# Kernel tuning notes

Measured on AMD Instinct MI355X. Metric: run time of the kernel, lower is better.

## Reference

```python
import jax, jax.numpy as jnp
import numpy as np

B, D_IN, D_BOT, C = 8192, 2048, 1024, 1000
SHARE = 500          # cfg.share_class_num
TEMP = 0.05          # cfg.temp
NEG_FILL = -1e9
EPS = 1e-12          # F.normalize eps


def setup_inputs() -> dict:
    key = jax.random.key(0)
    ks = jax.random.split(key, 6)
    return {
        "features": jax.random.normal(ks[0], (B, D_IN), jnp.float32),
        "W_b": jax.random.normal(ks[1], (D_BOT, D_IN), jnp.float32) * 0.02,
        "b_b": jnp.zeros((D_BOT,), jnp.float32),
        "W1": jax.random.normal(ks[2], (C, D_BOT), jnp.float32) * 0.02,
        "W2": jax.random.normal(ks[3], (C, D_BOT), jnp.float32) * 0.02,
        "centroid": jax.random.normal(ks[4], (C, D_BOT), jnp.float32) * 0.02,
    }


def mask_mechanism(outputs):
    # per-row mask: argmax -> row mask -> masked softmax (branchless)
    predict = jnp.argmax(outputs, axis=1)                       # [B]
    cls = jnp.arange(C)                                          # [C]
    base = cls < SHARE                                           # shared classes masked
    # if predicted class is private (>= SHARE), mask the whole row ...
    row_mask = jnp.where((predict >= SHARE)[:, None], True, base[None, :])
    # ... but always unmask the predicted class itself
    row_mask = row_mask & (cls[None, :] != predict[:, None])     # [B, C] bool
    masked = jnp.where(row_mask, jnp.float32(NEG_FILL), outputs)
    return jax.nn.softmax(masked, axis=1)


def reference(features, W_b, b_b, W1, W2, centroid):
    feats = features @ W_b.T + b_b                               # bottleneck [B, D_BOT]
    outputs1 = feats @ W1.T                                      # [B, C]
    sm1 = mask_mechanism(outputs1)
    feat_oa = sm1 @ centroid                                     # [B, D_BOT]
    features_aug = feats + feat_oa
    # F.normalize(dim=1): x / max(||x||_2, eps)
    norm = jnp.sqrt(jnp.sum(features_aug * features_aug, axis=1, keepdims=True))
    x = features_aug / jnp.maximum(norm, EPS)
    outputs2 = (x @ W2.T) / TEMP                                 # [B, C]
    softmax_outputs = jax.nn.softmax(outputs2, axis=1)
    return (feats, features_aug, outputs1, outputs2, softmax_outputs)
```

## Files before the change

kernel.cpp:

```cpp
#include <hip/hip_runtime.h>
#include <cmath>


typedef _Float16 h8 __attribute__((ext_vector_type(8)));
typedef _Float16 h4 __attribute__((ext_vector_type(4)));
typedef float f32x4 __attribute__((ext_vector_type(4)));

#define TAU 0.015f
#define CAP 1024

__device__ __forceinline__ void gload_lds16(const _Float16* g, _Float16* l) {
    __builtin_amdgcn_global_load_lds(
        (const __attribute__((address_space(1))) void*)g,
        (__attribute__((address_space(3))) void*)l, 16, 0, 0);
}

__global__ void zero_cnt_kernel(int* __restrict__ cnt) { *cnt = 0; }

template <int MODE>
__global__ __launch_bounds__(256, (MODE >= 5) ? 2 : 4) void gemm16(
    const _Float16* __restrict__ Ah, const _Float16* __restrict__ Al, int lda,
    const _Float16* __restrict__ Bh, const _Float16* __restrict__ Bl, int ldb,
    int klen,
    float* __restrict__ C, int ldc, int nC,
    const float* __restrict__ aux,
    _Float16* __restrict__ Ch,
    const int* __restrict__ cnt)
{
    constexpr bool P2 = (MODE >= 5);
    __shared__ _Float16 sAh[128 * 64];
    __shared__ _Float16 sBh[128 * 64];
    __shared__ _Float16 sAl[P2 ? 128 * 64 : 8];
    __shared__ _Float16 sBl[P2 ? 128 * 64 : 8];

    const int t = threadIdx.x;
    const int lane = t & 63, wid = t >> 6;
    int row0, col0, kbase;
    if constexpr (MODE >= 5) {
        row0 = blockIdx.y * 128; col0 = blockIdx.x * 128;
        kbase = blockIdx.z * klen;
        if (row0 >= *cnt) return;
    } else {
        const int wg = blockIdx.x;
        const int wgid = (wg & 7) * 64 + (wg >> 3);
        row0 = (wgid >> 3) * 128; col0 = (wgid & 7) * 128;
        kbase = 0;
    }
    const int wr = wid >> 1, wc = wid & 1;
    const int fr = lane & 15;
    const int fk = (lane >> 4) * 8;
    const int srow = lane >> 3;
    const int scol = (lane & 7) * 8;

    f32x4 acc[4][4] = {};
    f32x4 accc[4][4] = {};

    for (int k0 = kbase; k0 < kbase + klen; k0 += 64) {
        #pragma unroll
        for (int j = 0; j < 4; ++j) {
            int i = wid * 4 + j;
            int r = i * 8 + srow;
            const size_t ga = (size_t)(row0 + r) * lda + k0 + scol;
            const size_t gb = (size_t)(col0 + r) * ldb + k0 + scol;
            gload_lds16(Ah + ga, &sAh[i * 512]);
            gload_lds16(Bh + gb, &sBh[i * 512]);
            if constexpr (P2) {
                gload_lds16(Al + ga, &sAl[i * 512]);
                gload_lds16(Bl + gb, &sBl[i * 512]);
            }
        }
        __syncthreads();
        #pragma unroll
        for (int ks = 0; ks < 2; ++ks) {
            h8 ah[4], al[4];
            #pragma unroll
            for (int mf = 0; mf < 4; ++mf) {
                int rr = wr * 64 + mf * 16 + fr;
                ah[mf] = *(const h8*)&sAh[rr * 64 + ks * 32 + fk];
                if constexpr (P2) al[mf] = *(const h8*)&sAl[rr * 64 + ks * 32 + fk];
            }
            #pragma unroll
            for (int nf = 0; nf < 4; ++nf) {
                int cc = wc * 64 + nf * 16 + fr;
                h8 bh = *(const h8*)&sBh[cc * 64 + ks * 32 + fk];
                h8 bl;
                if constexpr (P2) bl = *(const h8*)&sBl[cc * 64 + ks * 32 + fk];
                #pragma unroll
                for (int mf = 0; mf < 4; ++mf) {
                    acc[mf][nf] = __builtin_amdgcn_mfma_f32_16x16x32_f16(ah[mf], bh, acc[mf][nf], 0, 0, 0);
                    if constexpr (P2) {
                        accc[mf][nf] = __builtin_amdgcn_mfma_f32_16x16x32_f16(ah[mf], bl, accc[mf][nf], 0, 0, 0);
                        accc[mf][nf] = __builtin_amdgcn_mfma_f32_16x16x32_f16(al[mf], bh, accc[mf][nf], 0, 0, 0);
                    }
                }
            }
        }
        __syncthreads();
    }
    float* Cz = C;
    if constexpr (MODE >= 5) Cz = C + (size_t)blockIdx.z * CAP * ldc;
    #pragma unroll
    for (int mf = 0; mf < 4; ++mf) {
        #pragma unroll
        for (int nf = 0; nf < 4; ++nf) {
            f32x4 v = acc[mf][nf];
            if constexpr (P2) v = v + accc[mf][nf] * (1.0f / 2048.0f);
            const int gcol = col0 + wc * 64 + nf * 16 + fr;
            const int rbase = row0 + wr * 64 + mf * 16 + (lane >> 4) * 4;
            #pragma unroll
            for (int j = 0; j < 4; ++j) {
                const int grow = rbase + j;
                float val = v[j];
                if constexpr (MODE == 1) val += aux[gcol];
                if constexpr (MODE == 3) val += aux[(size_t)grow * 1024 + gcol];
                if constexpr (MODE == 4) val *= 20.0f;
                if (gcol < nC) {
                    Cz[(size_t)grow * ldc + gcol] = val;
                    if constexpr (MODE == 1)
                        Ch[(size_t)grow * 1024 + gcol] = (_Float16)val;
                }
            }
        }
    }
}

__global__ void conv_kernel(const float* __restrict__ src, _Float16* __restrict__ hi, int n4)
{
    for (int i = blockIdx.x * 256 + threadIdx.x; i < n4; i += gridDim.x * 256) {
        f32x4 v = ((const f32x4*)src)[i];
        h4 h;
        #pragma unroll
        for (int j = 0; j < 4; ++j) h[j] = (_Float16)v[j];
        ((h4*)hi)[i] = h;
    }
}

__global__ void split_kernel(const float* __restrict__ src,
                             _Float16* __restrict__ hi, _Float16* __restrict__ lo, int n4)
{
    for (int i = blockIdx.x * 256 + threadIdx.x; i < n4; i += gridDim.x * 256) {
        f32x4 v = ((const f32x4*)src)[i];
        h4 h, l;
        #pragma unroll
        for (int j = 0; j < 4; ++j) {
            _Float16 hh = (_Float16)v[j];
            h[j] = hh;
            l[j] = (_Float16)((v[j] - (float)hh) * 2048.0f);
        }
        ((h4*)hi)[i] = h;
        ((h4*)lo)[i] = l;
    }
}

template <bool LO>
__global__ void padsplit_kernel(const float* __restrict__ src,
                                _Float16* __restrict__ hi, _Float16* __restrict__ lo, int nrows)
{
    for (int i = blockIdx.x * 256 + threadIdx.x; i < 1024 * 256; i += gridDim.x * 256) {
        int r = i >> 8;
        f32x4 v = {0.f, 0.f, 0.f, 0.f};
        if (r < nrows) v = ((const f32x4*)src)[i];
        h4 h, l;
        #pragma unroll
        for (int j = 0; j < 4; ++j) {
            _Float16 hh = (_Float16)v[j];
            h[j] = hh;
            if constexpr (LO) l[j] = (_Float16)((v[j] - (float)hh) * 2048.0f);
        }
        ((h4*)hi)[i] = h;
        if constexpr (LO) ((h4*)lo)[i] = l;
    }
}

__global__ __launch_bounds__(256) void ctrans_kernel(const float* __restrict__ centroid,
                                                     _Float16* __restrict__ cT)
{
    __shared__ float tile[32][33];
    const int t = threadIdx.x;
    const int tx = t & 31, ty = t >> 5;
    const int k0 = blockIdx.y * 32, n0 = blockIdx.x * 32;
    #pragma unroll
    for (int p = 0; p < 4; ++p) {
        int k = k0 + ty + p * 8;
        tile[ty + p * 8][tx] = (k < 1000) ? centroid[(size_t)k * 1024 + n0 + tx] : 0.0f;
    }
    __syncthreads();
    #pragma unroll
    for (int p = 0; p < 4; ++p) {
        int n = n0 + ty + p * 8;
        cT[(size_t)n * 1024 + k0 + tx] = (_Float16)tile[tx][ty + p * 8];
    }
}

__device__ __forceinline__ void masked_softmax_body(
    const float* __restrict__ x, _Float16* __restrict__ y,
    int t, float* wv, int* wi, bool flag, int* d_idx, int* d_cnt, int rowid)
{
    float bv = -1e30f, sv = -1e30f; int bi = 0;
    for (int c = t; c < 1000; c += 256) {
        float v = x[c];
        if (v > bv) { sv = bv; bv = v; bi = c; }
        else if (v > sv) sv = v;
    }
    #pragma unroll
    for (int off = 32; off > 0; off >>= 1) {
        float ov = __shfl_down(bv, off, 64);
        int   oi = __shfl_down(bi, off, 64);
        float os = __shfl_down(sv, off, 64);
        if (ov > bv || (ov == bv && oi < bi)) {
            sv = fmaxf(bv, os); bv = ov; bi = oi;
        } else {
            sv = fmaxf(sv, fmaxf(ov, os) == ov ? ov : os);
            sv = fmaxf(sv, ov); sv = fmaxf(sv, os);
        }
    }
    __shared__ float svv[4];
    const int lane = t & 63, wid = t >> 6;
    if (lane == 0) { wv[wid] = bv; wi[wid] = bi; svv[wid] = sv; }
    __syncthreads();
    __shared__ float s_m, s_tot; __shared__ int s_p;
    if (t == 0) {
        float mv = wv[0]; int mi = wi[0]; float m2 = svv[0];
        for (int w = 1; w < 4; ++w) {
            if (wv[w] > mv || (wv[w] == mv && wi[w] < mi)) {
                m2 = fmaxf(mv, svv[w]); mv = wv[w]; mi = wi[w];
            } else {
                m2 = fmaxf(m2, fmaxf(wv[w], svv[w]));
            }
        }
        s_p = mi; s_m = mv;
        if (flag && (mv - m2) < TAU) {
            int slot = atomicAdd(d_cnt, 1);
            if (slot < CAP) d_idx[slot] = rowid;
        }
    }
    __syncthreads();
    const int p = s_p; const float m = s_m;
    if (p >= 500) {
        for (int c = t; c < 1024; c += 256) y[c] = (c == p) ? (_Float16)1.0f : (_Float16)0.0f;
    } else {
        float s = 0.f;
        for (int c = t; c < 1000; c += 256)
            if (c == p || c >= 500) s += expf(x[c] - m);
        #pragma unroll
        for (int off = 32; off > 0; off >>= 1) s += __shfl_down(s, off, 64);
        if (lane == 0) wv[wid] = s;
        __syncthreads();
        if (t == 0) s_tot = wv[0] + wv[1] + wv[2] + wv[3];
        __syncthreads();
        const float inv = 1.0f / s_tot;
        for (int c = t; c < 1024; c += 256) {
            float v = 0.f;
            if (c < 1000 && (c == p || c >= 500)) v = expf(x[c] - m) * inv;
            y[c] = (_Float16)v;
        }
    }
}

__global__ __launch_bounds__(256) void masksm_kernel(const float* __restrict__ o1,
                                                     _Float16* __restrict__ sm,
                                                     int* __restrict__ d_idx,
                                                     int* __restrict__ d_cnt)
{
    __shared__ float wv[4]; __shared__ int wi[4];
    const int row = blockIdx.x;
    masked_softmax_body(o1 + (size_t)row * 1000, sm + (size_t)row * 1024,
                        threadIdx.x, wv, wi, true, d_idx, d_cnt, row);
}

__global__ __launch_bounds__(256) void fixup_kernel(const float* __restrict__ o1g,
                                                    _Float16* __restrict__ sm,
                                                    const int* __restrict__ d_idx,
                                                    const int* __restrict__ d_cnt)
{
    const int slot = blockIdx.x;
    if (slot >= *d_cnt || slot >= CAP) return;
    const int row = d_idx[slot];
    __shared__ float wv[4]; __shared__ int wi[4];
    masked_softmax_body(o1g + (size_t)slot * 1000, sm + (size_t)row * 1024,
                        threadIdx.x, wv, wi, false, nullptr, nullptr, 0);
}

__global__ __launch_bounds__(256) void gather_split_kernel(
    const float* __restrict__ features,
    _Float16* __restrict__ fgh, _Float16* __restrict__ fgl,
    const int* __restrict__ d_idx, const int* __restrict__ d_cnt)
{
    const int slot = blockIdx.x;
    if (slot >= *d_cnt || slot >= CAP) return;
    const int row = d_idx[slot];
    const int t = threadIdx.x;
    #pragma unroll
    for (int q = 0; q < 2; ++q) {
        int o = t * 8 + q * 4;
        f32x4 v = *(const f32x4*)(features + (size_t)row * 2048 + o);
        h4 h, l;
        #pragma unroll
        for (int j = 0; j < 4; ++j) {
            _Float16 hh = (_Float16)v[j];
            h[j] = hh;
            l[j] = (_Float16)((v[j] - (float)hh) * 2048.0f);
        }
        *(h4*)(fgh + (size_t)slot * 2048 + o) = h;
        *(h4*)(fgl + (size_t)slot * 2048 + o) = l;
    }
}

__global__ __launch_bounds__(256) void red1_kernel(const float* __restrict__ P1,
                                                   const float* __restrict__ bias,
                                                   _Float16* __restrict__ fgsh,
                                                   _Float16* __restrict__ fgsl,
                                                   const int* __restrict__ d_cnt)
{
    const int slot = blockIdx.x;
    if (slot >= *d_cnt || slot >= CAP) return;
    const int t = threadIdx.x;
    #pragma unroll
    for (int q = 0; q < 4; ++q) {
        const int c = t + q * 256;
        const size_t o = (size_t)slot * 1024 + c;
        float s = P1[o] + P1[o + (size_t)CAP * 1024] + P1[o + (size_t)2 * CAP * 1024]
                + P1[o + (size_t)3 * CAP * 1024] + bias[c];
        _Float16 h = (_Float16)s;
        fgsh[o] = h;
        fgsl[o] = (_Float16)((s - (float)h) * 2048.0f);
    }
}

__global__ __launch_bounds__(256) void red2_kernel(const float* __restrict__ P2,
                                                   float* __restrict__ o1g,
                                                   const int* __restrict__ d_cnt)
{
    const int slot = blockIdx.x;
    if (slot >= *d_cnt || slot >= CAP) return;
    const int t = threadIdx.x;
    for (int c = t; c < 1000; c += 256) {
        const size_t o = (size_t)slot * 1000 + c;
        o1g[o] = P2[o] + P2[o + (size_t)CAP * 1000];
    }
}

__global__ __launch_bounds__(256) void rownorm_x_kernel(const float* __restrict__ aug,
                                                        _Float16* __restrict__ xh)
{
    const int row = blockIdx.x; const int t = threadIdx.x;
    f32x4 v = *((const f32x4*)(aug + (size_t)row * 1024) + t);
    float s = v[0]*v[0] + v[1]*v[1] + v[2]*v[2] + v[3]*v[3];
    #pragma unroll
    for (int off = 32; off > 0; off >>= 1) s += __shfl_down(s, off, 64);
    __shared__ float ws4[4]; __shared__ float s_inv;
    const int lane = t & 63, wid = t >> 6;
    if (lane == 0) ws4[wid] = s;
    __syncthreads();
    if (t == 0) {
        float tot = ws4[0] + ws4[1] + ws4[2] + ws4[3];
        s_inv = 1.0f / fmaxf(sqrtf(tot), 1e-12f);
    }
    __syncthreads();
    const float inv = s_inv;
    h4 h;
    #pragma unroll
    for (int j = 0; j < 4; ++j) h[j] = (_Float16)(v[j] * inv);
    *((h4*)(xh + (size_t)row * 1024) + t) = h;
}

__global__ __launch_bounds__(256) void softmax2_kernel(const float* __restrict__ o2,
                                                       float* __restrict__ out)
{
    const int row = blockIdx.x; const int t = threadIdx.x;
    const float* x = o2 + (size_t)row * 1000;
    float* y = out + (size_t)row * 1000;
    float m = -1e30f;
    for (int c = t; c < 1000; c += 256) m = fmaxf(m, x[c]);
    #pragma unroll
    for (int off = 32; off > 0; off >>= 1) m = fmaxf(m, __shfl_down(m, off, 64));
    __shared__ float sm4[4]; __shared__ float s_m, s_s;
    const int lane = t & 63, wid = t >> 6;
    if (lane == 0) sm4[wid] = m;
    __syncthreads();
    if (t == 0) s_m = fmaxf(fmaxf(sm4[0], sm4[1]), fmaxf(sm4[2], sm4[3]));
    __syncthreads();
    m = s_m;
    float s = 0.f;
    for (int c = t; c < 1000; c += 256) s += expf(x[c] - m);
    #pragma unroll
    for (int off = 32; off > 0; off >>= 1) s += __shfl_down(s, off, 64);
    if (lane == 0) sm4[wid] = s;
    __syncthreads();
    if (t == 0) s_s = sm4[0] + sm4[1] + sm4[2] + sm4[3];
    __syncthreads();
    const float inv = 1.0f / s_s;
    for (int c = t; c < 1000; c += 256) y[c] = expf(x[c] - m) * inv;
}

extern "C" void kernel_launch(void* const* d_in, const int* in_sizes, int n_in,
                              void* d_out, int out_size, void* d_ws, size_t ws_size,
                              hipStream_t stream)
{
    const float* features = (const float*)d_in[0];
    const float* W_b      = (const float*)d_in[1];
    const float* b_b      = (const float*)d_in[2];
    const float* W1       = (const float*)d_in[3];
    const float* W2       = (const float*)d_in[4];
    const float* centroid = (const float*)d_in[5];

    char* base = (char*)d_out;
    float* feats = (float*)(base);
    float* aug   = (float*)(base + 33554432);
    float* o1    = (float*)(base + 67108864);
    float* o2    = (float*)(base + 99876864);
    float* smx   = (float*)(base + 132644864);

    _Float16* fh    = (_Float16*)(base + 67108864);
    _Float16* fetsh = (_Float16*)(base + 33554432);
    float*    P1    = (float*)   (base + 33554432);
    float*    P2    = (float*)   (base + 33554432);
    int*      idx   = (int*)     (base + 50331648);
    int*      cnt   = (int*)     (base + 50339840);
    _Float16* fgsh  = (_Float16*)(base + 50348032);
    _Float16* fgsl  = (_Float16*)(base + 52445184);
    float*    o1g   = (float*)   (base + 54542336);
    _Float16* sm1h  = (_Float16*)(base + 99876864);
    _Float16* cth   = (_Float16*)(base + 116654080);
    _Float16* wbh   = (_Float16*)(base + 118751232);
    _Float16* wbl   = (_Float16*)(base + 122945536);
    _Float16* w2h   = (_Float16*)(base + 132644864);
    _Float16* w1h   = (_Float16*)(base + 142606336);
    _Float16* w1l   = (_Float16*)(base + 144703488);
    _Float16* fgh   = (_Float16*)(base + 146800640);
    _Float16* fgl   = (_Float16*)(base + 150994944);
    _Float16* xh    = (_Float16*)(base + 146800640);

    zero_cnt_kernel<<<1, 1, 0, stream>>>(cnt);

    conv_kernel<<<2048, 256, 0, stream>>>(features, fh, 4194304);
    split_kernel<<<1024, 256, 0, stream>>>(W_b, wbh, wbl, 524288);
    padsplit_kernel<true><<<1024, 256, 0, stream>>>(W1, w1h, w1l, 1000);
    ctrans_kernel<<<dim3(32, 32), 256, 0, stream>>>(centroid, cth);
    padsplit_kernel<false><<<1024, 256, 0, stream>>>(W2, w2h, nullptr, 1000);

    gemm16<1><<<512, 256, 0, stream>>>(fh, nullptr, 2048, wbh, nullptr, 2048, 2048,
                                       feats, 1024, 1024, b_b, fetsh, nullptr);
    gemm16<2><<<512, 256, 0, stream>>>(fetsh, nullptr, 1024, w1h, nullptr, 1024, 1024,
                                       o1, 1000, 1000, nullptr, nullptr, nullptr);
    masksm_kernel<<<8192, 256, 0, stream>>>(o1, sm1h, idx, cnt);

    gather_split_kernel<<<CAP, 256, 0, stream>>>(features, fgh, fgl, idx, cnt);
    gemm16<5><<<dim3(8, CAP / 128, 4), 256, 0, stream>>>(fgh, fgl, 2048, wbh, wbl, 2048, 512,
                                                         P1, 1024, 1024, nullptr, nullptr, cnt);
    red1_kernel<<<CAP, 256, 0, stream>>>(P1, b_b, fgsh, fgsl, cnt);
    gemm16<5><<<dim3(8, CAP / 128, 2), 256, 0, stream>>>(fgsh, fgsl, 1024, w1h, w1l, 1024, 512,
                                                         P2, 1000, 1000, nullptr, nullptr, cnt);
    red2_kernel<<<CAP, 256, 0, stream>>>(P2, o1g, cnt);
    fixup_kernel<<<CAP, 256, 0, stream>>>(o1g, sm1h, idx, cnt);

    gemm16<3><<<512, 256, 0, stream>>>(sm1h, nullptr, 1024, cth, nullptr, 1024, 1024,
                                       aug, 1024, 1024, feats, nullptr, nullptr);
    rownorm_x_kernel<<<8192, 256, 0, stream>>>(aug, xh);
    gemm16<4><<<512, 256, 0, stream>>>(xh, nullptr, 1024, w2h, nullptr, 1024, 1024,
                                       o2, 1000, 1000, nullptr, nullptr, nullptr);
    softmax2_kernel<<<8192, 256, 0, stream>>>(o2, smx);
}
```

Before: 307.7 us.

## Add triple-buffered 256x128 GEMM with 8 waves and fuse split-K reduction into fixup

Replaces the four main fp16 GEMMs with a new kernel that uses 512 threads, 256x128 tiles and a three-stage LDS ring. Global-to-LDS loads for tile k+2 are interleaved with MFMA phases using explicit vmcnt waits, barriers and setprio. The dual-precision correction GEMM is split into its own non-templated kernel. The red2 split-K reduction is folded into fixup_kernel, which sums the partials into shared memory, removing one launch and one intermediate buffer. The new GEMM leaves room for only one block per CU and depends on hand-tuned waitcnt and barrier sequencing.

```diff
diff --git a/kernel.cpp b/kernel.cpp
--- a/kernel.cpp
+++ b/kernel.cpp
@@ -18,34 +18,130 @@
 __global__ void zero_cnt_kernel(int* __restrict__ cnt) { *cnt = 0; }
 
 template <int MODE>
-__global__ __launch_bounds__(256, (MODE >= 5) ? 2 : 4) void gemm16(
+__global__ __launch_bounds__(512, 1) void gemm8p(
+    const _Float16* __restrict__ Ah, int lda,
+    const _Float16* __restrict__ Bh, int ldb, int K,
+    float* __restrict__ C, int ldc, int nC,
+    const float* __restrict__ aux, _Float16* __restrict__ Ch)
+{
+    __shared__ _Float16 sA[3][256 * 64];
+    __shared__ _Float16 sB[3][128 * 64];
+
+    const int t = threadIdx.x;
+    const int lane = t & 63, wid = t >> 6;
+    const int wg = blockIdx.x;
+    const int wgid = (wg & 7) * 32 + (wg >> 3);
+    const int row0 = (wgid >> 3) * 256, col0 = (wgid & 7) * 128;
+    const int wr = wid >> 2, wc = wid & 3;
+    const int fr = lane & 15;
+    const int fk = (lane >> 4) * 8;
+    const int srow = lane >> 3;
+    const int scol = (lane & 7) * 8;
+
+    f32x4 acc[8][2] = {};
+
+    auto stage = [&](int b, int kt, int ph) {
+        const int kk = kt * 64;
+        if (ph == 0 || ph == 1) {
+            #pragma unroll
+            for (int j = 0; j < 2; ++j) {
+                const int i = wid * 4 + ph * 2 + j;
+                const int r = i * 8 + srow;
+                gload_lds16(Ah + (size_t)(row0 + r) * lda + kk + scol, &sA[b][i * 512]);
+            }
+        } else if (ph == 2) {
+            #pragma unroll
+            for (int j = 0; j < 2; ++j) {
+                const int i = wid * 2 + j;
+                const int r = i * 8 + srow;
+                gload_lds16(Bh + (size_t)(col0 + r) * ldb + kk + scol, &sB[b][i * 512]);
+            }
+        }
+    };
+
+    const int NT = K >> 6;
+    #pragma unroll
+    for (int ph = 0; ph < 3; ++ph) stage(0, 0, ph);
+    #pragma unroll
+    for (int ph = 0; ph < 3; ++ph) stage(1, 1, ph);
+    asm volatile("s_waitcnt vmcnt(6)" ::: "memory");
+    __builtin_amdgcn_s_barrier();
+
+    for (int kt = 0; kt < NT; ++kt) {
+        const int cb = kt % 3;
+        const int pb = (kt + 2) % 3;
+        const bool pf = (kt + 2) < NT;
+        h8 b0, b1;
+        #pragma unroll
+        for (int ph = 0; ph < 4; ++ph) {
+            const int ks = ph >> 1, mh = ph & 1;
+            if (mh == 0) {
+                b0 = *(const h8*)&sB[cb][(wc * 32 + fr) * 64 + ks * 32 + fk];
+                b1 = *(const h8*)&sB[cb][(wc * 32 + 16 + fr) * 64 + ks * 32 + fk];
+            }
+            h8 af[4];
+            #pragma unroll
+            for (int i = 0; i < 4; ++i)
+                af[i] = *(const h8*)&sA[cb][(wr * 128 + (mh * 4 + i) * 16 + fr) * 64 + ks * 32 + fk];
+            if (pf) stage(pb, kt + 2, ph);
+            if (ph == 3) {
+                if (pf)             asm volatile("s_waitcnt vmcnt(6)" ::: "memory");
+                else if (kt + 1 < NT) asm volatile("s_waitcnt vmcnt(0)" ::: "memory");
+            }
+            __builtin_amdgcn_s_barrier();
+            asm volatile("s_waitcnt lgkmcnt(0)" ::: "memory");
+            __builtin_amdgcn_s_setprio(1);
+            #pragma unroll
+            for (int i = 0; i < 4; ++i) {
+                acc[mh * 4 + i][0] = __builtin_amdgcn_mfma_f32_16x16x32_f16(af[i], b0, acc[mh * 4 + i][0], 0, 0, 0);
+                acc[mh * 4 + i][1] = __builtin_amdgcn_mfma_f32_16x16x32_f16(af[i], b1, acc[mh * 4 + i][1], 0, 0, 0);
+            }
+            __builtin_amdgcn_s_setprio(0);
+            __builtin_amdgcn_s_barrier();
+        }
+    }
+
+    #pragma unroll
+    for (int mf = 0; mf < 8; ++mf) {
+        #pragma unroll
+        for (int nf = 0; nf < 2; ++nf) {
+            f32x4 v = acc[mf][nf];
+            const int gcol = col0 + wc * 32 + nf * 16 + fr;
+            const int rbase = row0 + wr * 128 + mf * 16 + (lane >> 4) * 4;
+            #pragma unroll
+            for (int j = 0; j < 4; ++j) {
+                const int grow = rbase + j;
+                float val = v[j];
+                if constexpr (MODE == 1) val += aux[gcol];
+                if constexpr (MODE == 3) val += aux[(size_t)grow * 1024 + gcol];
+                if constexpr (MODE == 4) val *= 20.0f;
+                if (gcol < nC) {
+                    C[(size_t)grow * ldc + gcol] = val;
+                    if constexpr (MODE == 1)
+                        Ch[(size_t)grow * 1024 + gcol] = (_Float16)val;
+                }
+            }
+        }
+    }
+}
+
+__global__ __launch_bounds__(256, 2) void gemmc(
     const _Float16* __restrict__ Ah, const _Float16* __restrict__ Al, int lda,
     const _Float16* __restrict__ Bh, const _Float16* __restrict__ Bl, int ldb,
     int klen,
     float* __restrict__ C, int ldc, int nC,
-    const float* __restrict__ aux,
-    _Float16* __restrict__ Ch,
     const int* __restrict__ cnt)
 {
-    constexpr bool P2 = (MODE >= 5);
     __shared__ _Float16 sAh[128 * 64];
     __shared__ _Float16 sBh[128 * 64];
-    __shared__ _Float16 sAl[P2 ? 128 * 64 : 8];
-    __shared__ _Float16 sBl[P2 ? 128 * 64 : 8];
+    __shared__ _Float16 sAl[128 * 64];
+    __shared__ _Float16 sBl[128 * 64];
 
     const int t = threadIdx.x;
     const int lane = t & 63, wid = t >> 6;
-    int row0, col0, kbase;
-    if constexpr (MODE >= 5) {
-        row0 = blockIdx.y * 128; col0 = blockIdx.x * 128;
-        kbase = blockIdx.z * klen;
-        if (row0 >= *cnt) return;
-    } else {
-        const int wg = blockIdx.x;
-        const int wgid = (wg & 7) * 64 + (wg >> 3);
-        row0 = (wgid >> 3) * 128; col0 = (wgid & 7) * 128;
-        kbase = 0;
-    }
+    const int row0 = blockIdx.y * 128, col0 = blockIdx.x * 128;
+    const int kbase = blockIdx.z * klen;
+    if (row0 >= *cnt) return;
     const int wr = wid >> 1, wc = wid & 1;
     const int fr = lane & 15;
     const int fk = (lane >> 4) * 8;
@@ -64,10 +160,8 @@
             const size_t gb = (size_t)(col0 + r) * ldb + k0 + scol;
             gload_lds16(Ah + ga, &sAh[i * 512]);
             gload_lds16(Bh + gb, &sBh[i * 512]);
-            if constexpr (P2) {
-                gload_lds16(Al + ga, &sAl[i * 512]);
-                gload_lds16(Bl + gb, &sBl[i * 512]);
-            }
+            gload_lds16(Al + ga, &sAl[i * 512]);
+            gload_lds16(Bl + gb, &sBl[i * 512]);
         }
         __syncthreads();
         #pragma unroll
@@ -77,48 +171,34 @@
             for (int mf = 0; mf < 4; ++mf) {
                 int rr = wr * 64 + mf * 16 + fr;
                 ah[mf] = *(const h8*)&sAh[rr * 64 + ks * 32 + fk];
-                if constexpr (P2) al[mf] = *(const h8*)&sAl[rr * 64 + ks * 32 + fk];
+                al[mf] = *(const h8*)&sAl[rr * 64 + ks * 32 + fk];
             }
             #pragma unroll
             for (int nf = 0; nf < 4; ++nf) {
                 int cc = wc * 64 + nf * 16 + fr;
                 h8 bh = *(const h8*)&sBh[cc * 64 + ks * 32 + fk];
-                h8 bl;
-                if constexpr (P2) bl = *(const h8*)&sBl[cc * 64 + ks * 32 + fk];
+                h8 bl = *(const h8*)&sBl[cc * 64 + ks * 32 + fk];
                 #pragma unroll
                 for (int mf = 0; mf < 4; ++mf) {
-                    acc[mf][nf] = __builtin_amdgcn_mfma_f32_16x16x32_f16(ah[mf], bh, acc[mf][nf], 0, 0, 0);
-                    if constexpr (P2) {
-                        accc[mf][nf] = __builtin_amdgcn_mfma_f32_16x16x32_f16(ah[mf], bl, accc[mf][nf], 0, 0, 0);
-                        accc[mf][nf] = __builtin_amdgcn_mfma_f32_16x16x32_f16(al[mf], bh, accc[mf][nf], 0, 0, 0);
-                    }
+                    acc[mf][nf]  = __builtin_amdgcn_mfma_f32_16x16x32_f16(ah[mf], bh, acc[mf][nf], 0, 0, 0);
+                    accc[mf][nf] = __builtin_amdgcn_mfma_f32_16x16x32_f16(ah[mf], bl, accc[mf][nf], 0, 0, 0);
+                    accc[mf][nf] = __builtin_amdgcn_mfma_f32_16x16x32_f16(al[mf], bh, accc[mf][nf], 0, 0, 0);
                 }
             }
         }
         __syncthreads();
     }
-    float* Cz = C;
-    if constexpr (MODE >= 5) Cz = C + (size_t)blockIdx.z * CAP * ldc;
+    float* Cz = C + (size_t)blockIdx.z * CAP * ldc;
     #pragma unroll
     for (int mf = 0; mf < 4; ++mf) {
         #pragma unroll
         for (int nf = 0; nf < 4; ++nf) {
-            f32x4 v = acc[mf][nf];
-            if constexpr (P2) v = v + accc[mf][nf] * (1.0f / 2048.0f);
+            f32x4 v = acc[mf][nf] + accc[mf][nf] * (1.0f / 2048.0f);
             const int gcol = col0 + wc * 64 + nf * 16 + fr;
             const int rbase = row0 + wr * 64 + mf * 16 + (lane >> 4) * 4;
             #pragma unroll
             for (int j = 0; j < 4; ++j) {
-                const int grow = rbase + j;
-                float val = v[j];
-                if constexpr (MODE == 1) val += aux[gcol];
-                if constexpr (MODE == 3) val += aux[(size_t)grow * 1024 + gcol];
-                if constexpr (MODE == 4) val *= 20.0f;
-                if (gcol < nC) {
-                    Cz[(size_t)grow * ldc + gcol] = val;
-                    if constexpr (MODE == 1)
-                        Ch[(size_t)grow * 1024 + gcol] = (_Float16)val;
-                }
+                if (gcol < nC) Cz[(size_t)(rbase + j) * ldc + gcol] = v[j];
             }
         }
     }
@@ -268,7 +348,7 @@
                         threadIdx.x, wv, wi, true, d_idx, d_cnt, row);
 }
 
-__global__ __launch_bounds__(256) void fixup_kernel(const float* __restrict__ o1g,
+__global__ __launch_bounds__(256) void fixup_kernel(const float* __restrict__ P2,
                                                     _Float16* __restrict__ sm,
                                                     const int* __restrict__ d_idx,
                                                     const int* __restrict__ d_cnt)
@@ -276,9 +356,16 @@
     const int slot = blockIdx.x;
     if (slot >= *d_cnt || slot >= CAP) return;
     const int row = d_idx[slot];
+    const int t = threadIdx.x;
+    __shared__ float xr[1000];
+    for (int c = t; c < 1000; c += 256) {
+        const size_t o = (size_t)slot * 1000 + c;
+        xr[c] = P2[o] + P2[o + (size_t)CAP * 1000];
+    }
+    __syncthreads();
     __shared__ float wv[4]; __shared__ int wi[4];
-    masked_softmax_body(o1g + (size_t)slot * 1000, sm + (size_t)row * 1024,
-                        threadIdx.x, wv, wi, false, nullptr, nullptr, 0);
+    masked_softmax_body(xr, sm + (size_t)row * 1024,
+                        t, wv, wi, false, nullptr, nullptr, 0);
 }
 
 __global__ __launch_bounds__(256) void gather_split_kernel(
@@ -327,19 +414,6 @@
     }
 }
 
-__global__ __launch_bounds__(256) void red2_kernel(const float* __restrict__ P2,
-                                                   float* __restrict__ o1g,
-                                                   const int* __restrict__ d_cnt)
-{
-    const int slot = blockIdx.x;
-    if (slot >= *d_cnt || slot >= CAP) return;
-    const int t = threadIdx.x;
-    for (int c = t; c < 1000; c += 256) {
-        const size_t o = (size_t)slot * 1000 + c;
-        o1g[o] = P2[o] + P2[o + (size_t)CAP * 1000];
-    }
-}
-
 __global__ __launch_bounds__(256) void rownorm_x_kernel(const float* __restrict__ aug,
                                                         _Float16* __restrict__ xh)
 {
@@ -419,7 +493,6 @@
     int*      cnt   = (int*)     (base + 50339840);
     _Float16* fgsh  = (_Float16*)(base + 50348032);
     _Float16* fgsl  = (_Float16*)(base + 52445184);
-    float*    o1g   = (float*)   (base + 54542336);
     _Float16* sm1h  = (_Float16*)(base + 99876864);
     _Float16* cth   = (_Float16*)(base + 116654080);
     _Float16* wbh   = (_Float16*)(base + 118751232);
@@ -439,25 +512,24 @@
     ctrans_kernel<<<dim3(32, 32), 256, 0, stream>>>(centroid, cth);
     padsplit_kernel<false><<<1024, 256, 0, stream>>>(W2, w2h, nullptr, 1000);
 
-    gemm16<1><<<512, 256, 0, stream>>>(fh, nullptr, 2048, wbh, nullptr, 2048, 2048,
-                                       feats, 1024, 1024, b_b, fetsh, nullptr);
-    gemm16<2><<<512, 256, 0, stream>>>(fetsh, nullptr, 1024, w1h, nullptr, 1024, 1024,
-                                       o1, 1000, 1000, nullptr, nullptr, nullptr);
+    gemm8p<1><<<256, 512, 0, stream>>>(fh, 2048, wbh, 2048, 2048,
+                                       feats, 1024, 1024, b_b, fetsh);
+    gemm8p<2><<<256, 512, 0, stream>>>(fetsh, 1024, w1h, 1024, 1024,
+                                       o1, 1000, 1000, nullptr, nullptr);
     masksm_kernel<<<8192, 256, 0, stream>>>(o1, sm1h, idx, cnt);
 
     gather_split_kernel<<<CAP, 256, 0, stream>>>(features, fgh, fgl, idx, cnt);
-    gemm16<5><<<dim3(8, CAP / 128, 4), 256, 0, stream>>>(fgh, fgl, 2048, wbh, wbl, 2048, 512,
-                                                         P1, 1024, 1024, nullptr, nullptr, cnt);
+    gemmc<<<dim3(8, CAP / 128, 4), 256, 0, stream>>>(fgh, fgl, 2048, wbh, wbl, 2048, 512,
+                                                     P1, 1024, 1024, cnt);
     red1_kernel<<<CAP, 256, 0, stream>>>(P1, b_b, fgsh, fgsl, cnt);
-    gemm16<5><<<dim3(8, CAP / 128, 2), 256, 0, stream>>>(fgsh, fgsl, 1024, w1h, w1l, 1024, 512,
-                                                         P2, 1000, 1000, nullptr, nullptr, cnt);
-    red2_kernel<<<CAP, 256, 0, stream>>>(P2, o1g, cnt);
-    fixup_kernel<<<CAP, 256, 0, stream>>>(o1g, sm1h, idx, cnt);
-
-    gemm16<3><<<512, 256, 0, stream>>>(sm1h, nullptr, 1024, cth, nullptr, 1024, 1024,
-                                       aug, 1024, 1024, feats, nullptr, nullptr);
+    gemmc<<<dim3(8, CAP / 128, 2), 256, 0, stream>>>(fgsh, fgsl, 1024, w1h, w1l, 1024, 512,
+                                                     P2, 1000, 1000, cnt);
+    fixup_kernel<<<CAP, 256, 0, stream>>>(P2, sm1h, idx, cnt);
+
+    gemm8p<3><<<256, 512, 0, stream>>>(sm1h, 1024, cth, 1024, 1024,
+                                       aug, 1024, 1024, feats, nullptr);
     rownorm_x_kernel<<<8192, 256, 0, stream>>>(aug, xh);
-    gemm16<4><<<512, 256, 0, stream>>>(xh, nullptr, 1024, w2h, nullptr, 1024, 1024,
-                                       o2, 1000, 1000, nullptr, nullptr, nullptr);
+    gemm8p<4><<<256, 512, 0, stream>>>(xh, 1024, w2h, 1024, 1024,
+                                       o2, 1000, 1000, nullptr, nullptr);
     softmax2_kernel<<<8192, 256, 0, stream>>>(o2, smx);
 }
```

Result: no change. 311.9 us (+1.4%).
